# Kernel tuning notes

Hardware: AMD Instinct MI355X
Metric: run time of the kernel (lower is better)

The kernel has to match this reference:

```python
import jax, jax.numpy as jnp
import numpy as np

N_NODES = 50000
N_EDGES = 800000
VOCAB = 100000
EMB = 64
HID = 64
N_CLASSES = 10
N_GRAPHS = 512


def setup_inputs() -> dict:
    key = jax.random.key(0)
    ks = jax.random.split(key, 12)
    node_ids = jax.random.randint(ks[0], (N_NODES,), 0, VOCAB)
    edge_index = jax.random.randint(ks[1], (2, N_EDGES), 0, N_NODES)
    batch = jnp.sort(jax.random.randint(ks[2], (N_NODES,), 0, N_GRAPHS))
    emb = jax.random.normal(ks[3], (VOCAB, EMB), jnp.float32)
    s_e = 1.0 / np.sqrt(EMB)
    s_h = 1.0 / np.sqrt(HID)
    Wl0 = jax.random.normal(ks[4], (EMB, HID), jnp.float32) * s_e
    bl0 = jnp.zeros((HID,), jnp.float32)
    Wr0 = jax.random.normal(ks[5], (EMB, HID), jnp.float32) * s_e
    Wl1 = jax.random.normal(ks[6], (HID, HID), jnp.float32) * s_h
    bl1 = jnp.zeros((HID,), jnp.float32)
    Wr1 = jax.random.normal(ks[7], (HID, HID), jnp.float32) * s_h
    Wout = jax.random.normal(ks[8], (HID, N_CLASSES), jnp.float32) * s_h
    bout = jnp.zeros((N_CLASSES,), jnp.float32)
    return {"node_ids": node_ids, "edge_index": edge_index, "batch": batch,
            "emb": emb, "Wl0": Wl0, "bl0": bl0, "Wr0": Wr0,
            "Wl1": Wl1, "bl1": bl1, "Wr1": Wr1, "Wout": Wout, "bout": bout}


def _sage_conv(x, src, dst, Wl, bl, Wr):
    # PyG SAGEConv (aggr='mean'): out_i = lin_l(mean_{j in N(i)} x_j) + lin_r(x_i)
    msg = x[src]                                      # [E, d] gather
    s = jax.ops.segment_sum(msg, dst, num_segments=N_NODES)
    cnt = jax.ops.segment_sum(jnp.ones((msg.shape[0], 1), x.dtype), dst,
                              num_segments=N_NODES)
    mean = jnp.where(cnt > 0, s / jnp.maximum(cnt, 1), 0)
    return mean @ Wl + bl + x @ Wr


def reference(node_ids, edge_index, batch, emb, Wl0, bl0, Wr0, Wl1, bl1, Wr1, Wout, bout):
    x = emb[node_ids]                                  # [N, EMB]
    src, dst = edge_index[0], edge_index[1]
    x = jax.nn.relu(_sage_conv(x, src, dst, Wl0, bl0, Wr0))
    x = jax.nn.relu(_sage_conv(x, src, dst, Wl1, bl1, Wr1))
    # global_mean_pool over graph ids
    s = jax.ops.segment_sum(x, batch, num_segments=N_GRAPHS)
    cnt = jax.ops.segment_sum(jnp.ones((x.shape[0], 1), x.dtype), batch,
                              num_segments=N_GRAPHS)
    pooled = jnp.where(cnt > 0, s / jnp.maximum(cnt, 1), 0)   # [G, HID]
    return pooled @ Wout + bout                        # [G, N_CLASSES]
```

## Files before the change

kernel.cpp:

```cpp
#include <hip/hip_runtime.h>
#include <hip/hip_bf16.h>

#define N_NODES 50000
#define N_EDGES 800000
#define EMB 64
#define HID 64
#define N_CLASSES 10
#define N_GRAPHS 512

#define BKT_SHIFT 6
#define BKT_NODES 64
#define NB_BKT ((N_NODES + BKT_NODES - 1) / BKT_NODES)
#define BKT_CAP 1408
#define CNT_STRIDE 16
#define EB_CHUNK 4096
#define EB_BLOCKS ((N_EDGES + EB_CHUNK - 1) / EB_CHUNK)
#define XFORM_BLOCKS ((N_NODES + 63) / 64)
#define XPAD 68

#define ACC8(vv, A)                                                            \
    do {                                                                       \
        A[0] += __uint_as_float((vv).x << 16);                                 \
        A[1] += __uint_as_float((vv).x & 0xFFFF0000u);                         \
        A[2] += __uint_as_float((vv).y << 16);                                 \
        A[3] += __uint_as_float((vv).y & 0xFFFF0000u);                         \
        A[4] += __uint_as_float((vv).z << 16);                                 \
        A[5] += __uint_as_float((vv).z & 0xFFFF0000u);                         \
        A[6] += __uint_as_float((vv).w << 16);                                 \
        A[7] += __uint_as_float((vv).w & 0xFFFF0000u);                         \
    } while (0)

__device__ __forceinline__ void build_local_csr(
    int bucket, const int* __restrict__ cnt, const int* __restrict__ ebuf,
    unsigned short* lcsr, int* nhist, int* sval, int* sexcl, int* ncur) {
    int tid = threadIdx.x;
    int bs = bucket * BKT_CAP;
    int ne = min(cnt[bucket * CNT_STRIDE], BKT_CAP);
    if (tid < BKT_NODES) { nhist[tid] = 0; ncur[tid] = 0; }
    __syncthreads();
    for (int i = tid; i < ne; i += 256)
        atomicAdd(&nhist[ebuf[bs + i] >> 16], 1);
    __syncthreads();
    if (tid < 64) {
        int v = nhist[tid];
        int s = v;
#pragma unroll
        for (int off = 1; off < 64; off <<= 1) {
            int u = __shfl_up(s, off, 64);
            if (tid >= off) s += u;
        }
        sval[tid] = v;
        sexcl[tid] = s - v;
    }
    __syncthreads();
    for (int i = tid; i < ne; i += 256) {
        int p = ebuf[bs + i];
        int l = p >> 16;
        int r = atomicAdd(&ncur[l], 1);
        lcsr[sexcl[l] + r] = (unsigned short)(p & 0xFFFF);
    }
    __syncthreads();
}

__device__ __forceinline__ void agg2(
    int sA, int dA, int sB, int dB, int sl,
    const unsigned short* lcsr, const __hip_bfloat16* __restrict__ Pb,
    float oA[8], float oB[8]) {
    float a0[8], a1[8], b0[8], b1[8];
#pragma unroll
    for (int j = 0; j < 8; j++) { a0[j] = 0.f; a1[j] = 0.f; b0[j] = 0.f; b1[j] = 0.f; }
    int eA = sA + dA, eB = sB + dB;
    int pA = sA, pB = sB;
    while ((pA + 8 <= eA) && (pB + 8 <= eB)) {
        uint4 vA[8], vB[8];
#pragma unroll
        for (int j = 0; j < 8; j++)
            vA[j] = ((const uint4*)(Pb + (size_t)lcsr[pA + j] * 64))[sl];
#pragma unroll
        for (int j = 0; j < 8; j++)
            vB[j] = ((const uint4*)(Pb + (size_t)lcsr[pB + j] * 64))[sl];
#pragma unroll
        for (int j = 0; j < 8; j++) ACC8(vA[j], ((j & 1) ? a1 : a0));
#pragma unroll
        for (int j = 0; j < 8; j++) ACC8(vB[j], ((j & 1) ? b1 : b0));
        pA += 8; pB += 8;
    }
    while (pA + 8 <= eA) {
        uint4 v[8];
#pragma unroll
        for (int j = 0; j < 8; j++)
            v[j] = ((const uint4*)(Pb + (size_t)lcsr[pA + j] * 64))[sl];
#pragma unroll
        for (int j = 0; j < 8; j++) ACC8(v[j], ((j & 1) ? a1 : a0));
        pA += 8;
    }
    while (pB + 8 <= eB) {
        uint4 v[8];
#pragma unroll
        for (int j = 0; j < 8; j++)
            v[j] = ((const uint4*)(Pb + (size_t)lcsr[pB + j] * 64))[sl];
#pragma unroll
        for (int j = 0; j < 8; j++) ACC8(v[j], ((j & 1) ? b1 : b0));
        pB += 8;
    }
    for (; pA < eA; ++pA) {
        uint4 v = ((const uint4*)(Pb + (size_t)lcsr[pA] * 64))[sl];
        ACC8(v, a0);
    }
    for (; pB < eB; ++pB) {
        uint4 v = ((const uint4*)(Pb + (size_t)lcsr[pB] * 64))[sl];
        ACC8(v, b0);
    }
    float invA = (dA > 0) ? 1.0f / (float)dA : 0.0f;
    float invB = (dB > 0) ? 1.0f / (float)dB : 0.0f;
#pragma unroll
    for (int j = 0; j < 8; j++) {
        oA[j] = (a0[j] + a1[j]) * invA;
        oB[j] = (b0[j] + b1[j]) * invB;
    }
}

__device__ __forceinline__ void finish_row(int node, int sl,
                                           const float* __restrict__ H,
                                           float m[8], float* dst) {
    if (node < N_NODES) {
        size_t off = (size_t)node * 64 + sl * 8;
        float4 q0 = *(const float4*)&H[off];
        float4 q1 = *(const float4*)&H[off + 4];
        m[0] = fmaxf(m[0] + q0.x, 0.f);
        m[1] = fmaxf(m[1] + q0.y, 0.f);
        m[2] = fmaxf(m[2] + q0.z, 0.f);
        m[3] = fmaxf(m[3] + q0.w, 0.f);
        m[4] = fmaxf(m[4] + q1.x, 0.f);
        m[5] = fmaxf(m[5] + q1.y, 0.f);
        m[6] = fmaxf(m[6] + q1.z, 0.f);
        m[7] = fmaxf(m[7] + q1.w, 0.f);
    } else {
#pragma unroll
        for (int j = 0; j < 8; j++) m[j] = 0.f;
    }
    *(float4*)&dst[sl * 8] = make_float4(m[0], m[1], m[2], m[3]);
    *(float4*)&dst[sl * 8 + 4] = make_float4(m[4], m[5], m[6], m[7]);
}

__global__ __launch_bounds__(256) void k_combo(
    const int* __restrict__ esrc, const int* __restrict__ edst,
    int* __restrict__ cnt, int* __restrict__ ebuf,
    const int* __restrict__ ids, const float* __restrict__ emb,
    const float* __restrict__ Wl, const float* __restrict__ bl,
    const float* __restrict__ Wr,
    __hip_bfloat16* __restrict__ Pb, float* __restrict__ Qout) {
    __shared__ float sW[64 * 64];
    __shared__ float sX[64 * XPAD];
    int t = threadIdx.x;
    if (blockIdx.x < EB_BLOCKS) {
        int* h = (int*)sW;
        int* bbase = h + NB_BKT;
        int* cur = (int*)sX;
        for (int i = t; i < NB_BKT; i += 256) { h[i] = 0; cur[i] = 0; }
        __syncthreads();
        int base = blockIdx.x * EB_CHUNK;
        int end = min(base + EB_CHUNK, N_EDGES);
        for (int i = base + t; i < end; i += 256)
            atomicAdd(&h[edst[i] >> BKT_SHIFT], 1);
        __syncthreads();
        for (int i = t; i < NB_BKT; i += 256)
            if (h[i]) bbase[i] = i * BKT_CAP + atomicAdd(&cnt[i * CNT_STRIDE], h[i]);
        __syncthreads();
        for (int i = base + t; i < end; i += 256) {
            int d = edst[i], s = esrc[i];
            int b = d >> BKT_SHIFT;
            int r = atomicAdd(&cur[b], 1);
            int slot = bbase[b] + r;
            if (slot < (b + 1) * BKT_CAP)
                ebuf[slot] = ((d & (BKT_NODES - 1)) << 16) | s;
        }
        return;
    }
    int tile = (blockIdx.x - EB_BLOCKS) * 64;
    for (int i = t; i < 64 * 16; i += 256)
        ((float4*)sW)[i] = ((const float4*)Wl)[i];
    for (int i = t; i < 64 * 16; i += 256) {
        int r = i >> 4, c = i & 15;
        int node = tile + r;
        float4 v = make_float4(0.f, 0.f, 0.f, 0.f);
        if (node < N_NODES)
            v = ((const float4*)(emb + (size_t)ids[node] * 64))[c];
        *(float4*)&sX[r * XPAD + c * 4] = v;
    }
    __syncthreads();
    int dg = t & 15, ng = t >> 4;
    float acc[4][4];
#pragma unroll
    for (int i = 0; i < 4; i++)
#pragma unroll
        for (int j = 0; j < 4; j++) acc[i][j] = 0.f;
#pragma unroll 4
    for (int k = 0; k < 64; k++) {
        float4 w = *(const float4*)&sW[k * 64 + dg * 4];
#pragma unroll
        for (int i = 0; i < 4; i++) {
            float xv = sX[(ng + i * 16) * XPAD + k];
            acc[i][0] = fmaf(xv, w.x, acc[i][0]);
            acc[i][1] = fmaf(xv, w.y, acc[i][1]);
            acc[i][2] = fmaf(xv, w.z, acc[i][2]);
            acc[i][3] = fmaf(xv, w.w, acc[i][3]);
        }
    }
#pragma unroll
    for (int i = 0; i < 4; i++) {
        int node = tile + ng + i * 16;
        if (node < N_NODES) {
            union { ushort4 u; __hip_bfloat16 h[4]; } pk;
            pk.h[0] = __float2bfloat16(acc[i][0]);
            pk.h[1] = __float2bfloat16(acc[i][1]);
            pk.h[2] = __float2bfloat16(acc[i][2]);
            pk.h[3] = __float2bfloat16(acc[i][3]);
            *(ushort4*)&Pb[(size_t)node * 64 + dg * 4] = pk.u;
        }
    }
    __syncthreads();
    for (int i = t; i < 64 * 16; i += 256)
        ((float4*)sW)[i] = ((const float4*)Wr)[i];
    __syncthreads();
#pragma unroll
    for (int i = 0; i < 4; i++)
#pragma unroll
        for (int j = 0; j < 4; j++) acc[i][j] = 0.f;
#pragma unroll 4
    for (int k = 0; k < 64; k++) {
        float4 w = *(const float4*)&sW[k * 64 + dg * 4];
#pragma unroll
        for (int i = 0; i < 4; i++) {
            float xv = sX[(ng + i * 16) * XPAD + k];
            acc[i][0] = fmaf(xv, w.x, acc[i][0]);
            acc[i][1] = fmaf(xv, w.y, acc[i][1]);
            acc[i][2] = fmaf(xv, w.z, acc[i][2]);
            acc[i][3] = fmaf(xv, w.w, acc[i][3]);
        }
    }
    float4 blv = *(const float4*)&bl[dg * 4];
#pragma unroll
    for (int i = 0; i < 4; i++) {
        int node = tile + ng + i * 16;
        if (node < N_NODES)
            *(float4*)&Qout[(size_t)node * 64 + dg * 4] =
                make_float4(acc[i][0] + blv.x, acc[i][1] + blv.y,
                            acc[i][2] + blv.z, acc[i][3] + blv.w);
    }
}

__global__ __launch_bounds__(256, 4) void k_fused1(
    const int* __restrict__ cnt, const int* __restrict__ ebuf,
    const __hip_bfloat16* __restrict__ Pb0, const float* __restrict__ Wl,
    const float* __restrict__ bl, const float* __restrict__ Wr,
    __hip_bfloat16* __restrict__ Pb1, float* __restrict__ H) {
    __shared__ float sW[64 * 64];
    __shared__ float sX[64 * XPAD];
    __shared__ unsigned short lcsr[BKT_CAP];
    __shared__ int nhist[BKT_NODES], sval[BKT_NODES], sexcl[BKT_NODES], ncur[BKT_NODES];
    int t = threadIdx.x;
    int tile = blockIdx.x * 64;
    for (int i = t; i < 64 * 16; i += 256)
        ((float4*)sW)[i] = ((const float4*)Wl)[i];
    build_local_csr(blockIdx.x, cnt, ebuf, lcsr, nhist, sval, sexcl, ncur);
    int grp = t >> 3, sl = t & 7;
    int ln0 = grp * 2, ln1 = ln0 + 1;
    float mA[8], mB[8];
    agg2(sexcl[ln0], sval[ln0], sexcl[ln1], sval[ln1], sl, lcsr, Pb0, mA, mB);
    finish_row(tile + ln0, sl, H, mA, &sX[ln0 * XPAD]);
    finish_row(tile + ln1, sl, H, mB, &sX[ln1 * XPAD]);
    __syncthreads();
    int dg = t & 15, ng = t >> 4;
    float acc[4][4];
#pragma unroll
    for (int i = 0; i < 4; i++)
#pragma unroll
        for (int j = 0; j < 4; j++) acc[i][j] = 0.f;
#pragma unroll 4
    for (int k = 0; k < 64; k++) {
        float4 w = *(const float4*)&sW[k * 64 + dg * 4];
#pragma unroll
        for (int i = 0; i < 4; i++) {
            float xv = sX[(ng + i * 16) * XPAD + k];
            acc[i][0] = fmaf(xv, w.x, acc[i][0]);
            acc[i][1] = fmaf(xv, w.y, acc[i][1]);
            acc[i][2] = fmaf(xv, w.z, acc[i][2]);
            acc[i][3] = fmaf(xv, w.w, acc[i][3]);
        }
    }
#pragma unroll
    for (int i = 0; i < 4; i++) {
        int node = tile + ng + i * 16;
        if (node < N_NODES) {
            union { ushort4 u; __hip_bfloat16 h[4]; } pk;
            pk.h[0] = __float2bfloat16(acc[i][0]);
            pk.h[1] = __float2bfloat16(acc[i][1]);
            pk.h[2] = __float2bfloat16(acc[i][2]);
            pk.h[3] = __float2bfloat16(acc[i][3]);
            *(ushort4*)&Pb1[(size_t)node * 64 + dg * 4] = pk.u;
        }
    }
    __syncthreads();
    for (int i = t; i < 64 * 16; i += 256)
        ((float4*)sW)[i] = ((const float4*)Wr)[i];
    __syncthreads();
#pragma unroll
    for (int i = 0; i < 4; i++)
#pragma unroll
        for (int j = 0; j < 4; j++) acc[i][j] = 0.f;
#pragma unroll 4
    for (int k = 0; k < 64; k++) {
        float4 w = *(const float4*)&sW[k * 64 + dg * 4];
#pragma unroll
        for (int i = 0; i < 4; i++) {
            float xv = sX[(ng + i * 16) * XPAD + k];
            acc[i][0] = fmaf(xv, w.x, acc[i][0]);
            acc[i][1] = fmaf(xv, w.y, acc[i][1]);
            acc[i][2] = fmaf(xv, w.z, acc[i][2]);
            acc[i][3] = fmaf(xv, w.w, acc[i][3]);
        }
    }
    float4 blv = *(const float4*)&bl[dg * 4];
#pragma unroll
    for (int i = 0; i < 4; i++) {
        int node = tile + ng + i * 16;
        if (node < N_NODES)
            *(float4*)&H[(size_t)node * 64 + dg * 4] =
                make_float4(acc[i][0] + blv.x, acc[i][1] + blv.y,
                            acc[i][2] + blv.z, acc[i][3] + blv.w);
    }
}

__global__ __launch_bounds__(256, 4) void k_agg2_pool(
    const int* __restrict__ cnt, const int* __restrict__ ebuf,
    const __hip_bfloat16* __restrict__ Pb, const float* __restrict__ H,
    const int* __restrict__ batch, float* __restrict__ psum) {
    __shared__ float sPool[64 * 64];
    __shared__ unsigned short lcsr[BKT_CAP];
    __shared__ int nhist[BKT_NODES], sval[BKT_NODES], sexcl[BKT_NODES], ncur[BKT_NODES];
    __shared__ int sLg[64];
    int t = threadIdx.x;
    int nb = blockIdx.x * 64;
    int gmin = batch[nb];
    if (t < 64) {
        int node = nb + t;
        sLg[t] = batch[node < N_NODES ? node : (N_NODES - 1)] - gmin;
    }
    build_local_csr(blockIdx.x, cnt, ebuf, lcsr, nhist, sval, sexcl, ncur);
    int grp = t >> 3, sl = t & 7;
    int ln0 = grp * 2, ln1 = ln0 + 1;
    float mA[8], mB[8];
    agg2(sexcl[ln0], sval[ln0], sexcl[ln1], sval[ln1], sl, lcsr, Pb, mA, mB);
    finish_row(nb + ln0, sl, H, mA, &sPool[ln0 * 64]);
    finish_row(nb + ln1, sl, H, mB, &sPool[ln1 * 64]);
    __syncthreads();
    int d = t & 63, q = t >> 6;
    int n0 = q * 16;
    float run = 0.f;
    int cur = sLg[n0];
    for (int n = n0; n < n0 + 16; n++) {
        int lg = sLg[n];
        if (lg != cur) {
            if (run != 0.f)
                atomicAdd(&psum[(size_t)(gmin + cur) * 64 + d], run);
            run = 0.f;
            cur = lg;
        }
        run += sPool[n * 64 + d];
    }
    if (run != 0.f)
        atomicAdd(&psum[(size_t)(gmin + cur) * 64 + d], run);
}

__device__ __forceinline__ int lower_bound_batch(const int* __restrict__ batch, int val) {
    int lo = 0, hi = N_NODES;
    while (lo < hi) {
        int mid = (lo + hi) >> 1;
        if (batch[mid] < val) lo = mid + 1; else hi = mid;
    }
    return lo;
}

__global__ __launch_bounds__(256) void k_out(
    const int* __restrict__ batch, const float* __restrict__ psum,
    const float* __restrict__ Wout, const float* __restrict__ bout,
    float* __restrict__ out) {
    int w = threadIdx.x >> 6, lane = threadIdx.x & 63;
    int g = blockIdx.x * 4 + w;
    if (g >= N_GRAPHS) return;
    int s0 = lower_bound_batch(batch, g);
    int s1 = lower_bound_batch(batch, g + 1);
    int cntg = s1 - s0;
    float inv = (cntg > 0) ? 1.0f / (float)cntg : 0.0f;
    float pooled = psum[(size_t)g * 64 + lane] * inv;
#pragma unroll
    for (int c = 0; c < N_CLASSES; c++) {
        float v = pooled * Wout[lane * N_CLASSES + c];
#pragma unroll
        for (int off = 32; off > 0; off >>= 1) v += __shfl_down(v, off, 64);
        if (lane == 0) out[(size_t)g * N_CLASSES + c] = v + bout[c];
    }
}


extern "C" void kernel_launch(void* const* d_in, const int* in_sizes, int n_in,
                              void* d_out, int out_size, void* d_ws, size_t ws_size,
                              hipStream_t stream) {
    const int*   node_ids = (const int*)d_in[0];
    const int*   edge_idx = (const int*)d_in[1];
    const int*   batch    = (const int*)d_in[2];
    const float* emb      = (const float*)d_in[3];
    const float* Wl0      = (const float*)d_in[4];
    const float* bl0      = (const float*)d_in[5];
    const float* Wr0      = (const float*)d_in[6];
    const float* Wl1      = (const float*)d_in[7];
    const float* bl1      = (const float*)d_in[8];
    const float* Wr1      = (const float*)d_in[9];
    const float* Wout     = (const float*)d_in[10];
    const float* bout     = (const float*)d_in[11];
    float* out = (float*)d_out;

    const int* esrc = edge_idx;
    const int* edst = edge_idx + N_EDGES;

    __hip_bfloat16* Pb0 = (__hip_bfloat16*)d_ws;
    __hip_bfloat16* Pb1 = Pb0 + (size_t)N_NODES * 64;
    float* H = (float*)(Pb1 + (size_t)N_NODES * 64);
    int* ebuf = (int*)(H + (size_t)N_NODES * 64);
    int* cnt = ebuf + (size_t)NB_BKT * BKT_CAP;
    float* psum = (float*)(cnt + (size_t)NB_BKT * CNT_STRIDE);

    const int BLK = 256;

    hipMemsetAsync(cnt, 0, (NB_BKT * CNT_STRIDE + N_GRAPHS * 64) * sizeof(int), stream);

    k_combo<<<EB_BLOCKS + XFORM_BLOCKS, BLK, 0, stream>>>(
        esrc, edst, cnt, ebuf, node_ids, emb, Wl0, bl0, Wr0, Pb0, H);

    k_fused1<<<XFORM_BLOCKS, BLK, 0, stream>>>(cnt, ebuf, Pb0, Wl1, bl1, Wr1, Pb1, H);

    k_agg2_pool<<<NB_BKT, BLK, 0, stream>>>(cnt, ebuf, Pb1, H, batch, psum);

    k_out<<<(N_GRAPHS + 3) / 4, BLK, 0, stream>>>(batch, psum, Wout, bout, out);
}
```

Baseline: 190.1 us.

## Fuse all stages into one persistent cooperative kernel with grid syncs

Replaces the memset and four separate kernel launches with a single cooperative persistent kernel. It zeroes the counters in-kernel, then runs each stage (bucket split plus layer-0 transform, layer-1 fused aggregation, layer-2 aggregation plus pooling, output head) separated by grid.sync. Each stage hands out work units through atomic work-queue counters. The aim is to remove launch and inter-kernel gaps and to balance uneven bucket work. In exchange it adds grid-wide barrier costs and may reduce occupancy because every block reserves the union of all stages' shared memory. The old multi-kernel path is kept as a fallback if the cooperative launch fails.

```diff
diff --git a/kernel.cpp b/kernel.cpp
--- a/kernel.cpp
+++ b/kernel.cpp
@@ -1,5 +1,8 @@
 #include <hip/hip_runtime.h>
 #include <hip/hip_bf16.h>
+#include <hip/hip_cooperative_groups.h>
+
+namespace cg = cooperative_groups;
 
 #define N_NODES 50000
 #define N_EDGES 800000
@@ -143,52 +146,10 @@
     *(float4*)&dst[sl * 8 + 4] = make_float4(m[4], m[5], m[6], m[7]);
 }
 
-__global__ __launch_bounds__(256) void k_combo(
-    const int* __restrict__ esrc, const int* __restrict__ edst,
-    int* __restrict__ cnt, int* __restrict__ ebuf,
-    const int* __restrict__ ids, const float* __restrict__ emb,
-    const float* __restrict__ Wl, const float* __restrict__ bl,
-    const float* __restrict__ Wr,
+__device__ __forceinline__ void two_gemm_from_sX(
+    int tile, int t, float* sW, const float* sX,
+    const float* __restrict__ Wr, const float* __restrict__ bl,
     __hip_bfloat16* __restrict__ Pb, float* __restrict__ Qout) {
-    __shared__ float sW[64 * 64];
-    __shared__ float sX[64 * XPAD];
-    int t = threadIdx.x;
-    if (blockIdx.x < EB_BLOCKS) {
-        int* h = (int*)sW;
-        int* bbase = h + NB_BKT;
-        int* cur = (int*)sX;
-        for (int i = t; i < NB_BKT; i += 256) { h[i] = 0; cur[i] = 0; }
-        __syncthreads();
-        int base = blockIdx.x * EB_CHUNK;
-        int end = min(base + EB_CHUNK, N_EDGES);
-        for (int i = base + t; i < end; i += 256)
-            atomicAdd(&h[edst[i] >> BKT_SHIFT], 1);
-        __syncthreads();
-        for (int i = t; i < NB_BKT; i += 256)
-            if (h[i]) bbase[i] = i * BKT_CAP + atomicAdd(&cnt[i * CNT_STRIDE], h[i]);
-        __syncthreads();
-        for (int i = base + t; i < end; i += 256) {
-            int d = edst[i], s = esrc[i];
-            int b = d >> BKT_SHIFT;
-            int r = atomicAdd(&cur[b], 1);
-            int slot = bbase[b] + r;
-            if (slot < (b + 1) * BKT_CAP)
-                ebuf[slot] = ((d & (BKT_NODES - 1)) << 16) | s;
-        }
-        return;
-    }
-    int tile = (blockIdx.x - EB_BLOCKS) * 64;
-    for (int i = t; i < 64 * 16; i += 256)
-        ((float4*)sW)[i] = ((const float4*)Wl)[i];
-    for (int i = t; i < 64 * 16; i += 256) {
-        int r = i >> 4, c = i & 15;
-        int node = tile + r;
-        float4 v = make_float4(0.f, 0.f, 0.f, 0.f);
-        if (node < N_NODES)
-            v = ((const float4*)(emb + (size_t)ids[node] * 64))[c];
-        *(float4*)&sX[r * XPAD + c * 4] = v;
-    }
-    __syncthreads();
     int dg = t & 15, ng = t >> 4;
     float acc[4][4];
 #pragma unroll
@@ -250,20 +211,63 @@
     }
 }
 
-__global__ __launch_bounds__(256, 4) void k_fused1(
-    const int* __restrict__ cnt, const int* __restrict__ ebuf,
+__device__ __forceinline__ void unit_bsplit(
+    int u, int t, const int* __restrict__ esrc, const int* __restrict__ edst,
+    int* __restrict__ cnt, int* __restrict__ ebuf, float* sW, float* sX) {
+    int* h = (int*)sW;
+    int* bbase = h + NB_BKT;
+    int* cur = (int*)sX;
+    for (int i = t; i < NB_BKT; i += 256) { h[i] = 0; cur[i] = 0; }
+    __syncthreads();
+    int base = u * EB_CHUNK;
+    int end = min(base + EB_CHUNK, N_EDGES);
+    for (int i = base + t; i < end; i += 256)
+        atomicAdd(&h[edst[i] >> BKT_SHIFT], 1);
+    __syncthreads();
+    for (int i = t; i < NB_BKT; i += 256)
+        if (h[i]) bbase[i] = i * BKT_CAP + atomicAdd(&cnt[i * CNT_STRIDE], h[i]);
+    __syncthreads();
+    for (int i = base + t; i < end; i += 256) {
+        int d = edst[i], s = esrc[i];
+        int b = d >> BKT_SHIFT;
+        int r = atomicAdd(&cur[b], 1);
+        int slot = bbase[b] + r;
+        if (slot < (b + 1) * BKT_CAP)
+            ebuf[slot] = ((d & (BKT_NODES - 1)) << 16) | s;
+    }
+}
+
+__device__ __forceinline__ void unit_xform0(
+    int tileIdx, int t, const int* __restrict__ ids, const float* __restrict__ emb,
+    const float* __restrict__ Wl, const float* __restrict__ bl,
+    const float* __restrict__ Wr, __hip_bfloat16* __restrict__ Pb,
+    float* __restrict__ Qout, float* sW, float* sX) {
+    int tile = tileIdx * 64;
+    for (int i = t; i < 64 * 16; i += 256)
+        ((float4*)sW)[i] = ((const float4*)Wl)[i];
+    for (int i = t; i < 64 * 16; i += 256) {
+        int r = i >> 4, c = i & 15;
+        int node = tile + r;
+        float4 v = make_float4(0.f, 0.f, 0.f, 0.f);
+        if (node < N_NODES)
+            v = ((const float4*)(emb + (size_t)ids[node] * 64))[c];
+        *(float4*)&sX[r * XPAD + c * 4] = v;
+    }
+    __syncthreads();
+    two_gemm_from_sX(tile, t, sW, sX, Wr, bl, Pb, Qout);
+}
+
+__device__ __forceinline__ void unit_fused1(
+    int u, int t, const int* __restrict__ cnt, const int* __restrict__ ebuf,
     const __hip_bfloat16* __restrict__ Pb0, const float* __restrict__ Wl,
     const float* __restrict__ bl, const float* __restrict__ Wr,
-    __hip_bfloat16* __restrict__ Pb1, float* __restrict__ H) {
-    __shared__ float sW[64 * 64];
-    __shared__ float sX[64 * XPAD];
-    __shared__ unsigned short lcsr[BKT_CAP];
-    __shared__ int nhist[BKT_NODES], sval[BKT_NODES], sexcl[BKT_NODES], ncur[BKT_NODES];
-    int t = threadIdx.x;
-    int tile = blockIdx.x * 64;
+    __hip_bfloat16* __restrict__ Pb1, float* __restrict__ H,
+    float* sW, float* sX, unsigned short* lcsr,
+    int* nhist, int* sval, int* sexcl, int* ncur) {
+    int tile = u * 64;
     for (int i = t; i < 64 * 16; i += 256)
         ((float4*)sW)[i] = ((const float4*)Wl)[i];
-    build_local_csr(blockIdx.x, cnt, ebuf, lcsr, nhist, sval, sexcl, ncur);
+    build_local_csr(u, cnt, ebuf, lcsr, nhist, sval, sexcl, ncur);
     int grp = t >> 3, sl = t & 7;
     int ln0 = grp * 2, ln1 = ln0 + 1;
     float mA[8], mB[8];
@@ -271,83 +275,22 @@
     finish_row(tile + ln0, sl, H, mA, &sX[ln0 * XPAD]);
     finish_row(tile + ln1, sl, H, mB, &sX[ln1 * XPAD]);
     __syncthreads();
-    int dg = t & 15, ng = t >> 4;
-    float acc[4][4];
-#pragma unroll
-    for (int i = 0; i < 4; i++)
-#pragma unroll
-        for (int j = 0; j < 4; j++) acc[i][j] = 0.f;
-#pragma unroll 4
-    for (int k = 0; k < 64; k++) {
-        float4 w = *(const float4*)&sW[k * 64 + dg * 4];
-#pragma unroll
-        for (int i = 0; i < 4; i++) {
-            float xv = sX[(ng + i * 16) * XPAD + k];
-            acc[i][0] = fmaf(xv, w.x, acc[i][0]);
-            acc[i][1] = fmaf(xv, w.y, acc[i][1]);
-            acc[i][2] = fmaf(xv, w.z, acc[i][2]);
-            acc[i][3] = fmaf(xv, w.w, acc[i][3]);
-        }
-    }
-#pragma unroll
-    for (int i = 0; i < 4; i++) {
-        int node = tile + ng + i * 16;
-        if (node < N_NODES) {
-            union { ushort4 u; __hip_bfloat16 h[4]; } pk;
-            pk.h[0] = __float2bfloat16(acc[i][0]);
-            pk.h[1] = __float2bfloat16(acc[i][1]);
-            pk.h[2] = __float2bfloat16(acc[i][2]);
-            pk.h[3] = __float2bfloat16(acc[i][3]);
-            *(ushort4*)&Pb1[(size_t)node * 64 + dg * 4] = pk.u;
-        }
-    }
-    __syncthreads();
-    for (int i = t; i < 64 * 16; i += 256)
-        ((float4*)sW)[i] = ((const float4*)Wr)[i];
-    __syncthreads();
-#pragma unroll
-    for (int i = 0; i < 4; i++)
-#pragma unroll
-        for (int j = 0; j < 4; j++) acc[i][j] = 0.f;
-#pragma unroll 4
-    for (int k = 0; k < 64; k++) {
-        float4 w = *(const float4*)&sW[k * 64 + dg * 4];
-#pragma unroll
-        for (int i = 0; i < 4; i++) {
-            float xv = sX[(ng + i * 16) * XPAD + k];
-            acc[i][0] = fmaf(xv, w.x, acc[i][0]);
-            acc[i][1] = fmaf(xv, w.y, acc[i][1]);
-            acc[i][2] = fmaf(xv, w.z, acc[i][2]);
-            acc[i][3] = fmaf(xv, w.w, acc[i][3]);
-        }
-    }
-    float4 blv = *(const float4*)&bl[dg * 4];
-#pragma unroll
-    for (int i = 0; i < 4; i++) {
-        int node = tile + ng + i * 16;
-        if (node < N_NODES)
-            *(float4*)&H[(size_t)node * 64 + dg * 4] =
-                make_float4(acc[i][0] + blv.x, acc[i][1] + blv.y,
-                            acc[i][2] + blv.z, acc[i][3] + blv.w);
-    }
-}
-
-__global__ __launch_bounds__(256, 4) void k_agg2_pool(
-    const int* __restrict__ cnt, const int* __restrict__ ebuf,
+    two_gemm_from_sX(tile, t, sW, sX, Wr, bl, Pb1, H);
+}
+
+__device__ __forceinline__ void unit_agg2pool(
+    int u, int t, const int* __restrict__ cnt, const int* __restrict__ ebuf,
     const __hip_bfloat16* __restrict__ Pb, const float* __restrict__ H,
-    const int* __restrict__ batch, float* __restrict__ psum) {
-    __shared__ float sPool[64 * 64];
-    __shared__ unsigned short lcsr[BKT_CAP];
-    __shared__ int nhist[BKT_NODES], sval[BKT_NODES], sexcl[BKT_NODES], ncur[BKT_NODES];
-    __shared__ int sLg[64];
-    int t = threadIdx.x;
-    int nb = blockIdx.x * 64;
+    const int* __restrict__ batch, float* __restrict__ psum,
+    float* sPool, unsigned short* lcsr,
+    int* nhist, int* sval, int* sexcl, int* ncur, int* sLg) {
+    int nb = u * 64;
     int gmin = batch[nb];
     if (t < 64) {
         int node = nb + t;
         sLg[t] = batch[node < N_NODES ? node : (N_NODES - 1)] - gmin;
     }
-    build_local_csr(blockIdx.x, cnt, ebuf, lcsr, nhist, sval, sexcl, ncur);
+    build_local_csr(u, cnt, ebuf, lcsr, nhist, sval, sexcl, ncur);
     int grp = t >> 3, sl = t & 7;
     int ln0 = grp * 2, ln1 = ln0 + 1;
     float mA[8], mB[8];
@@ -380,6 +323,131 @@
         if (batch[mid] < val) lo = mid + 1; else hi = mid;
     }
     return lo;
+}
+
+__global__ __launch_bounds__(256, 4) void k_all(
+    const int* __restrict__ esrc, const int* __restrict__ edst,
+    int* __restrict__ cnt, int* __restrict__ ebuf,
+    const int* __restrict__ ids, const float* __restrict__ emb,
+    const float* __restrict__ Wl0, const float* __restrict__ bl0,
+    const float* __restrict__ Wr0,
+    __hip_bfloat16* __restrict__ Pb0, float* __restrict__ H,
+    const float* __restrict__ Wl1, const float* __restrict__ bl1,
+    const float* __restrict__ Wr1, __hip_bfloat16* __restrict__ Pb1,
+    const int* __restrict__ batch, float* __restrict__ psum,
+    int* __restrict__ wq,
+    const float* __restrict__ Wout, const float* __restrict__ bout,
+    float* __restrict__ out) {
+    cg::grid_group grid = cg::this_grid();
+    __shared__ float sW[64 * 64];
+    __shared__ float sX[64 * XPAD];
+    __shared__ unsigned short lcsr[BKT_CAP];
+    __shared__ int nhist[BKT_NODES], sval[BKT_NODES], sexcl[BKT_NODES], ncur[BKT_NODES];
+    __shared__ int sLg[BKT_NODES];
+    __shared__ int sU;
+    int t = threadIdx.x;
+
+    {
+        int4* zb = (int4*)cnt;
+        const int zi4 = (NB_BKT * CNT_STRIDE + N_GRAPHS * 64 + 8) >> 2;
+        for (int i = blockIdx.x * 256 + t; i < zi4; i += gridDim.x * 256)
+            zb[i] = make_int4(0, 0, 0, 0);
+    }
+    grid.sync();
+
+    const int NU_A = EB_BLOCKS + XFORM_BLOCKS;
+    for (;;) {
+        __syncthreads();
+        if (t == 0) sU = atomicAdd(&wq[0], 1);
+        __syncthreads();
+        int u = sU;
+        if (u >= NU_A) break;
+        if (u < EB_BLOCKS)
+            unit_bsplit(u, t, esrc, edst, cnt, ebuf, sW, sX);
+        else
+            unit_xform0(u - EB_BLOCKS, t, ids, emb, Wl0, bl0, Wr0, Pb0, H, sW, sX);
+    }
+    grid.sync();
+
+    for (;;) {
+        __syncthreads();
+        if (t == 0) sU = atomicAdd(&wq[1], 1);
+        __syncthreads();
+        int u = sU;
+        if (u >= NB_BKT) break;
+        unit_fused1(u, t, cnt, ebuf, Pb0, Wl1, bl1, Wr1, Pb1, H,
+                    sW, sX, lcsr, nhist, sval, sexcl, ncur);
+    }
+    grid.sync();
+
+    for (;;) {
+        __syncthreads();
+        if (t == 0) sU = atomicAdd(&wq[2], 1);
+        __syncthreads();
+        int u = sU;
+        if (u >= NB_BKT) break;
+        unit_agg2pool(u, t, cnt, ebuf, Pb1, H, batch, psum,
+                      sW, lcsr, nhist, sval, sexcl, ncur, sLg);
+    }
+    grid.sync();
+
+    int w = t >> 6, lane = t & 63;
+    for (int g = blockIdx.x * 4 + w; g < N_GRAPHS; g += gridDim.x * 4) {
+        int s0 = lower_bound_batch(batch, g);
+        int s1 = lower_bound_batch(batch, g + 1);
+        int cntg = s1 - s0;
+        float inv = (cntg > 0) ? 1.0f / (float)cntg : 0.0f;
+        float pooled = psum[(size_t)g * 64 + lane] * inv;
+#pragma unroll
+        for (int c = 0; c < N_CLASSES; c++) {
+            float v = pooled * Wout[lane * N_CLASSES + c];
+#pragma unroll
+            for (int off = 32; off > 0; off >>= 1) v += __shfl_down(v, off, 64);
+            if (lane == 0) out[(size_t)g * N_CLASSES + c] = v + bout[c];
+        }
+    }
+}
+
+__global__ __launch_bounds__(256) void k_combo(
+    const int* __restrict__ esrc, const int* __restrict__ edst,
+    int* __restrict__ cnt, int* __restrict__ ebuf,
+    const int* __restrict__ ids, const float* __restrict__ emb,
+    const float* __restrict__ Wl, const float* __restrict__ bl,
+    const float* __restrict__ Wr,
+    __hip_bfloat16* __restrict__ Pb, float* __restrict__ Qout) {
+    __shared__ float sW[64 * 64];
+    __shared__ float sX[64 * XPAD];
+    int t = threadIdx.x;
+    if (blockIdx.x < EB_BLOCKS) {
+        unit_bsplit(blockIdx.x, t, esrc, edst, cnt, ebuf, sW, sX);
+        return;
+    }
+    unit_xform0(blockIdx.x - EB_BLOCKS, t, ids, emb, Wl, bl, Wr, Pb, Qout, sW, sX);
+}
+
+__global__ __launch_bounds__(256, 4) void k_fused1(
+    const int* __restrict__ cnt, const int* __restrict__ ebuf,
+    const __hip_bfloat16* __restrict__ Pb0, const float* __restrict__ Wl,
+    const float* __restrict__ bl, const float* __restrict__ Wr,
+    __hip_bfloat16* __restrict__ Pb1, float* __restrict__ H) {
+    __shared__ float sW[64 * 64];
+    __shared__ float sX[64 * XPAD];
+    __shared__ unsigned short lcsr[BKT_CAP];
+    __shared__ int nhist[BKT_NODES], sval[BKT_NODES], sexcl[BKT_NODES], ncur[BKT_NODES];
+    unit_fused1(blockIdx.x, threadIdx.x, cnt, ebuf, Pb0, Wl, bl, Wr, Pb1, H,
+                sW, sX, lcsr, nhist, sval, sexcl, ncur);
+}
+
+__global__ __launch_bounds__(256, 4) void k_agg2_pool(
+    const int* __restrict__ cnt, const int* __restrict__ ebuf,
+    const __hip_bfloat16* __restrict__ Pb, const float* __restrict__ H,
+    const int* __restrict__ batch, float* __restrict__ psum) {
+    __shared__ float sPool[64 * 64];
+    __shared__ unsigned short lcsr[BKT_CAP];
+    __shared__ int nhist[BKT_NODES], sval[BKT_NODES], sexcl[BKT_NODES], ncur[BKT_NODES];
+    __shared__ int sLg[64];
+    unit_agg2pool(blockIdx.x, threadIdx.x, cnt, ebuf, Pb, H, batch, psum,
+                  sPool, lcsr, nhist, sval, sexcl, ncur, sLg);
 }
 
 __global__ __launch_bounds__(256) void k_out(
@@ -430,17 +498,39 @@
     int* ebuf = (int*)(H + (size_t)N_NODES * 64);
     int* cnt = ebuf + (size_t)NB_BKT * BKT_CAP;
     float* psum = (float*)(cnt + (size_t)NB_BKT * CNT_STRIDE);
+    int* wq = (int*)(psum + (size_t)N_GRAPHS * 64);
 
     const int BLK = 256;
 
-    hipMemsetAsync(cnt, 0, (NB_BKT * CNT_STRIDE + N_GRAPHS * 64) * sizeof(int), stream);
-
-    k_combo<<<EB_BLOCKS + XFORM_BLOCKS, BLK, 0, stream>>>(
-        esrc, edst, cnt, ebuf, node_ids, emb, Wl0, bl0, Wr0, Pb0, H);
-
-    k_fused1<<<XFORM_BLOCKS, BLK, 0, stream>>>(cnt, ebuf, Pb0, Wl1, bl1, Wr1, Pb1, H);
-
-    k_agg2_pool<<<NB_BKT, BLK, 0, stream>>>(cnt, ebuf, Pb1, H, batch, psum);
-
-    k_out<<<(N_GRAPHS + 3) / 4, BLK, 0, stream>>>(batch, psum, Wout, bout, out);
-}
+    static int s_grid = -1;
+    if (s_grid < 0) {
+        int nb = 0;
+        if (hipOccupancyMaxActiveBlocksPerMultiprocessor(&nb, k_all, BLK, 0)
+                != hipSuccess || nb < 1)
+            nb = 0;
+        s_grid = nb * 256;
+        if (s_grid > EB_BLOCKS + XFORM_BLOCKS) s_grid = EB_BLOCKS + XFORM_BLOCKS;
+    }
+
+    bool ok = false;
+    if (s_grid >= 256) {
+        void* args[] = {(void*)&esrc, (void*)&edst, (void*)&cnt, (void*)&ebuf,
+                        (void*)&node_ids, (void*)&emb, (void*)&Wl0, (void*)&bl0,
+                        (void*)&Wr0, (void*)&Pb0, (void*)&H, (void*)&Wl1,
+                        (void*)&bl1, (void*)&Wr1, (void*)&Pb1, (void*)&batch,
+                        (void*)&psum, (void*)&wq, (void*)&Wout, (void*)&bout,
+                        (void*)&out};
+        ok = (hipLaunchCooperativeKernel(k_all, dim3(s_grid), dim3(BLK),
+                                         args, 0, stream) == hipSuccess);
+    }
+    if (!ok) {
+        hipMemsetAsync(cnt, 0, (NB_BKT * CNT_STRIDE + N_GRAPHS * 64) * sizeof(int),
+                       stream);
+        k_combo<<<EB_BLOCKS + XFORM_BLOCKS, BLK, 0, stream>>>(
+            esrc, edst, cnt, ebuf, node_ids, emb, Wl0, bl0, Wr0, Pb0, H);
+        k_fused1<<<XFORM_BLOCKS, BLK, 0, stream>>>(cnt, ebuf, Pb0, Wl1, bl1, Wr1,
+                                                   Pb1, H);
+        k_agg2_pool<<<NB_BKT, BLK, 0, stream>>>(cnt, ebuf, Pb1, H, batch, psum);
+        k_out<<<(N_GRAPHS + 3) / 4, BLK, 0, stream>>>(batch, psum, Wout, bout, out);
+    }
+}
```

Result: slower. 460.6 us (+142.3%).
